# Kernel tuning notes

Hardware: AMD Instinct MI355X
Metric: run time of the kernel (lower is better)

Reference implementation:

```python
import jax, jax.numpy as jnp
import numpy as np

B, C, D, H, W = 4, 64, 64, 64, 64
EPS = 1e-5

def setup_inputs() -> dict:
    key = jax.random.key(0)
    ks = jax.random.split(key, 10)
    s = 1.0 / np.sqrt(C)
    so = 1.0 / np.sqrt(D)
    return {
        "x": jax.random.normal(ks[0], (B, C, H, W), jnp.float32),
        "gn_weight": jnp.ones((C,), jnp.float32),
        "gn_bias": jnp.zeros((C,), jnp.float32),
        "wq": jax.random.uniform(ks[1], (D, C), jnp.float32, -s, s),
        "bq": jax.random.uniform(ks[2], (D,), jnp.float32, -s, s),
        "wk": jax.random.uniform(ks[3], (D, C), jnp.float32, -s, s),
        "bk": jax.random.uniform(ks[4], (D,), jnp.float32, -s, s),
        "wv": jax.random.uniform(ks[5], (D, C), jnp.float32, -s, s),
        "bv": jax.random.uniform(ks[6], (D,), jnp.float32, -s, s),
        "wo": jax.random.uniform(ks[7], (D, D), jnp.float32, -so, so),
        "bo": jax.random.uniform(ks[8], (D,), jnp.float32, -so, so),
    }

def reference(x, gn_weight, gn_bias, wq, bq, wk, bk, wv, bv, wo, bo):
    # GroupNorm with num_groups == channels: per (batch, channel) norm over H,W
    mu = jnp.mean(x, axis=(2, 3), keepdims=True)
    var = jnp.var(x, axis=(2, 3), keepdims=True)
    xn = (x - mu) * jax.lax.rsqrt(var + EPS)
    xn = xn * gn_weight[None, :, None, None] + gn_bias[None, :, None, None]

    # 1x1 convs == channel matmuls; flatten spatial: bcn
    xf = xn.reshape(B, C, H * W)
    Q = jnp.einsum('dc,bcn->bdn', wq, xf) + bq[None, :, None]
    K = jnp.einsum('dc,bcn->bdn', wk, xf) + bk[None, :, None]
    V = jnp.einsum('dc,bcn->bdn', wv, xf) + bv[None, :, None]

    scale = 1.0 / jnp.sqrt(jnp.asarray(D, x.dtype))
    aff = jnp.einsum('bdn,bdm->bnm', Q, K) * scale  # [B, N, N]
    aff = jax.nn.softmax(aff, axis=2)
    att = jnp.einsum('bnm,bdm->bdn', aff, V)  # [B, D, N]

    out = jnp.einsum('ed,bdn->ben', wo, att) + bo[None, :, None]
    return out.reshape(B, D, H, W)
```

## Files before the change

### kernel.cpp

```cpp
#include <hip/hip_runtime.h>


#define B_ 4
#define C_ 64
#define D_ 64
#define N_ 4096

using bf16x8 = __attribute__((ext_vector_type(8))) short;
using u16x8  = __attribute__((ext_vector_type(8))) unsigned short;
using u32x4  = __attribute__((ext_vector_type(4))) unsigned int;
using f32x16 = __attribute__((ext_vector_type(16))) float;

__device__ __forceinline__ unsigned short f2bf(float f) {
    unsigned u = __builtin_bit_cast(unsigned, f);
    u = (u + 0x7FFFu + ((u >> 16) & 1u)) >> 16;
    return (unsigned short)u;
}

#if __has_builtin(__builtin_amdgcn_exp2f)
__device__ __forceinline__ float fast_exp2(float x) {
    return __builtin_amdgcn_exp2f(x);
}
#else
__device__ __forceinline__ float fast_exp2(float x) {
    float r;
    asm volatile("v_exp_f32 %0, %1\n\ts_nop 1" : "=v"(r) : "v"(x));
    return r;
}
#endif

__device__ __forceinline__ void gload16(const void* g, void* l) {
    __builtin_amdgcn_global_load_lds(
        (const __attribute__((address_space(1))) unsigned int*)g,
        (__attribute__((address_space(3))) unsigned int*)l, 16, 0, 0);
}

__global__ __launch_bounds__(1024)
void gn_stats_kernel(const float* __restrict__ x, float* __restrict__ stats) {
    __shared__ float red[32];
    const int bx  = blockIdx.x;
    const int tid = threadIdx.x;
    const float4* xp = (const float4*)(x + (size_t)bx * N_);
    float4 v = xp[tid];
    float s = (v.x + v.y) + (v.z + v.w);
    float q = (v.x * v.x + v.y * v.y) + (v.z * v.z + v.w * v.w);
#pragma unroll
    for (int off = 1; off < 64; off <<= 1) {
        s += __shfl_xor(s, off);
        q += __shfl_xor(q, off);
    }
    const int w = tid >> 6;
    if ((tid & 63) == 0) { red[w * 2] = s; red[w * 2 + 1] = q; }
    __syncthreads();
    if (w == 0) {
        const int lane = tid & 63;
        float sl = (lane < 16) ? red[lane * 2] : 0.f;
        float ql = (lane < 16) ? red[lane * 2 + 1] : 0.f;
#pragma unroll
        for (int off = 1; off < 16; off <<= 1) {
            sl += __shfl_xor(sl, off);
            ql += __shfl_xor(ql, off);
        }
        if (lane == 0) {
            float mu  = sl * (1.f / 4096.f);
            float var = ql * (1.f / 4096.f) - mu * mu;
            var = fmaxf(var, 0.f);
            stats[bx * 2]     = mu;
            stats[bx * 2 + 1] = 1.f / sqrtf(var + 1e-5f);
        }
    }
}

__global__ __launch_bounds__(512)
void gn_qkv_kernel(const float* __restrict__ x, const float* __restrict__ stats,
                   const float* __restrict__ gnw, const float* __restrict__ gnb,
                   const float* __restrict__ wq, const float* __restrict__ bq,
                   const float* __restrict__ wk, const float* __restrict__ bk,
                   const float* __restrict__ wv, const float* __restrict__ bv,
                   unsigned short* __restrict__ Qt, unsigned short* __restrict__ Kf,
                   unsigned short* __restrict__ Vf) {
    __shared__ float xn[64 * 64];
    __shared__ __align__(16) char vs[64 * 128];
    const int t  = threadIdx.x;
    const int bx = blockIdx.x;
    const int b  = bx >> 6;
    const int n0 = (bx & 63) * 64;

    {
        const int c  = t >> 3;
        const int nc = (t & 7) * 8;
        const float* xp = x + (size_t)(b * 64 + c) * N_ + n0 + nc;
        float4 xa = *(const float4*)(xp);
        float4 xb = *(const float4*)(xp + 4);
        float mu = stats[(b * 64 + c) * 2];
        float rs = stats[(b * 64 + c) * 2 + 1];
        float gw = gnw[c] * rs;
        float gb = gnb[c] - mu * gw;
        float* xr = xn + c * 64 + nc;
        xr[0] = xa.x * gw + gb; xr[1] = xa.y * gw + gb;
        xr[2] = xa.z * gw + gb; xr[3] = xa.w * gw + gb;
        xr[4] = xb.x * gw + gb; xr[5] = xb.y * gw + gb;
        xr[6] = xb.z * gw + gb; xr[7] = xb.w * gw + gb;
    }
    __syncthreads();

    const int n    = t & 63;
    const int dblk = __builtin_amdgcn_readfirstlane(t >> 6);
    const int d0   = dblk * 8;

    float aq[8], ak[8], av[8];
#pragma unroll
    for (int i = 0; i < 8; ++i) { aq[i] = 0.f; ak[i] = 0.f; av[i] = 0.f; }

#pragma unroll 4
    for (int c = 0; c < 64; ++c) {
        const float xv = xn[c * 64 + n];
#pragma unroll
        for (int i = 0; i < 8; ++i) {
            aq[i] += wq[(d0 + i) * 64 + c] * xv;
            ak[i] += wk[(d0 + i) * 64 + c] * xv;
            av[i] += wv[(d0 + i) * 64 + c] * xv;
        }
    }

    const float QS = 0.18033688011112042f;
    const int m = n0 + n;
    u16x8 qv, kv, vb;
#pragma unroll
    for (int i = 0; i < 8; ++i) {
        qv[i] = f2bf((aq[i] + bq[d0 + i]) * QS);
        kv[i] = f2bf(ak[i] + bk[d0 + i]);
        vb[i] = f2bf(av[i] + bv[d0 + i]);
    }
    *(u16x8*)(Qt + ((size_t)(b * N_ + m)) * 64 + d0) = qv;
    {
        const int kc = dblk >> 1, h = dblk & 1, mt = m >> 5;
        *(u16x8*)(Kf + ((size_t)((b * 128 + mt) * 4 + kc)) * 512
                     + (h * 32 + (m & 31)) * 8) = kv;
    }
    *(u16x8*)(vs + n * 128 + ((dblk * 16) ^ ((n & 7) << 4))) = vb;
    __syncthreads();

    {
        const int mc_l = t >> 7;
        const int dt   = (t >> 6) & 1;
        const int lp   = t & 63;
        const int hp   = lp >> 5;
        const int dcol = (lp & 31) + dt * 32;
        const int cbase = (dcol & ~7) * 2;
        const int clow  = (dcol & 7) * 2;
        u16x8 tmp;
#pragma unroll
        for (int j = 0; j < 8; ++j) {
            const int ml = mc_l * 16 + hp * 8 + j;
            tmp[j] = *(const unsigned short*)(
                vs + ml * 128 + (cbase ^ (j << 4)) + clow);
        }
        *(u16x8*)(Vf + ((size_t)((b * 256 + (n0 >> 4) + mc_l) * 2 + dt)) * 512
                     + lp * 8) = tmp;
    }
}

__global__ __launch_bounds__(512, 2)
void attn_kernel(const unsigned short* __restrict__ Qt,
                 const unsigned short* __restrict__ Kf,
                 const unsigned short* __restrict__ Vf,
                 const float* __restrict__ wo, const float* __restrict__ bo,
                 float* __restrict__ out) {
    __shared__ __align__(16) char smem[131072];
    const int tid  = threadIdx.x;
    const int lane = tid & 63;
    const int wvu  = __builtin_amdgcn_readfirstlane(tid >> 6);
    const int c    = lane & 31;
    const int h    = lane >> 5;
    const int bid  = blockIdx.x;
    const int b    = bid & 3;
    const int qc   = bid >> 2;
    const int n0   = qc * 64;

    const unsigned short* qp = Qt + (size_t)(b * N_ + n0 + c) * 64 + h * 8;
    bf16x8 qa0[4], qa1[4];
#pragma unroll
    for (int kc = 0; kc < 4; ++kc) {
        qa0[kc] = *(const bf16x8*)(qp + kc * 16);
        qa1[kc] = *(const bf16x8*)(qp + 32 * 64 + kc * 16);
    }

    f32x16 o00, o01, o10, o11;
#pragma unroll
    for (int i = 0; i < 16; ++i) { o00[i] = 0.f; o01[i] = 0.f; o10[i] = 0.f; o11[i] = 0.f; }
    float lsA0 = 0.f, lsA1 = 0.f, lsB0 = 0.f, lsB1 = 0.f;

    const int lof = lane * 16;
    char* sbase = smem + wvu * 16384;
    const char* kTn = (const char*)Kf + (size_t)b * 524288 + (size_t)wvu * 65536;
    const char* vTn = (const char*)Vf + (size_t)b * 524288 + (size_t)wvu * 65536;

#pragma unroll
    for (int j = 0; j < 4; ++j) {
        gload16(kTn + j * 1024 + lof, sbase + j * 1024);
        gload16(vTn + j * 1024 + lof, sbase + 4096 + j * 1024);
    }
    asm volatile("s_waitcnt vmcnt(0)" ::: "memory");
    __builtin_amdgcn_sched_barrier(0);

    for (int t = 0; t < 16; ++t) {
        char* buf = sbase + ((t & 1) << 13);
        if (t + 1 < 16) {
            kTn += 4096;
            vTn += 4096;
            char* dst = sbase + (((t & 1) ^ 1) << 13);
#pragma unroll
            for (int j = 0; j < 4; ++j) {
                gload16(kTn + j * 1024 + lof, dst + j * 1024);
                gload16(vTn + j * 1024 + lof, dst + 4096 + j * 1024);
            }
        }

        const char* kb = buf + lof;
        bf16x8 kf0 = *(const bf16x8*)(kb);
        bf16x8 kf1 = *(const bf16x8*)(kb + 1024);
        bf16x8 kf2 = *(const bf16x8*)(kb + 2048);
        bf16x8 kf3 = *(const bf16x8*)(kb + 3072);
        f32x16 sa0, sa1;
#pragma unroll
        for (int i = 0; i < 16; ++i) { sa0[i] = 0.f; sa1[i] = 0.f; }
        sa0 = __builtin_amdgcn_mfma_f32_32x32x16_bf16(kf0, qa0[0], sa0, 0, 0, 0);
        sa1 = __builtin_amdgcn_mfma_f32_32x32x16_bf16(kf0, qa1[0], sa1, 0, 0, 0);
        sa0 = __builtin_amdgcn_mfma_f32_32x32x16_bf16(kf1, qa0[1], sa0, 0, 0, 0);
        sa1 = __builtin_amdgcn_mfma_f32_32x32x16_bf16(kf1, qa1[1], sa1, 0, 0, 0);
        sa0 = __builtin_amdgcn_mfma_f32_32x32x16_bf16(kf2, qa0[2], sa0, 0, 0, 0);
        sa1 = __builtin_amdgcn_mfma_f32_32x32x16_bf16(kf2, qa1[2], sa1, 0, 0, 0);
        sa0 = __builtin_amdgcn_mfma_f32_32x32x16_bf16(kf3, qa0[3], sa0, 0, 0, 0);
        sa1 = __builtin_amdgcn_mfma_f32_32x32x16_bf16(kf3, qa1[3], sa1, 0, 0, 0);

#pragma unroll
        for (int i = 0; i < 16; i += 2) {
            float pA0 = fast_exp2(sa0[i]);
            float pA1 = fast_exp2(sa0[i + 1]);
            float pB0 = fast_exp2(sa1[i]);
            float pB1 = fast_exp2(sa1[i + 1]);
            sa0[i] = pA0; sa0[i + 1] = pA1;
            sa1[i] = pB0; sa1[i + 1] = pB1;
            lsA0 += pA0; lsA1 += pA1;
            lsB0 += pB0; lsB1 += pB1;
        }
        unsigned dwa[8], dwb[8];
#pragma unroll
        for (int i = 0; i < 8; ++i) {
            asm("v_cvt_pk_bf16_f32 %0, %1, %2"
                : "=v"(dwa[i]) : "v"(sa0[2 * i]), "v"(sa0[2 * i + 1]));
            asm("v_cvt_pk_bf16_f32 %0, %1, %2"
                : "=v"(dwb[i]) : "v"(sa1[2 * i]), "v"(sa1[2 * i + 1]));
        }
        asm("v_permlane32_swap_b32 %0, %1" : "+v"(dwa[0]), "+v"(dwa[2]));
        asm("v_permlane32_swap_b32 %0, %1" : "+v"(dwa[1]), "+v"(dwa[3]));
        asm("v_permlane32_swap_b32 %0, %1" : "+v"(dwa[4]), "+v"(dwa[6]));
        asm("v_permlane32_swap_b32 %0, %1" : "+v"(dwa[5]), "+v"(dwa[7]));
        asm("v_permlane32_swap_b32 %0, %1" : "+v"(dwb[0]), "+v"(dwb[2]));
        asm("v_permlane32_swap_b32 %0, %1" : "+v"(dwb[1]), "+v"(dwb[3]));
        asm("v_permlane32_swap_b32 %0, %1" : "+v"(dwb[4]), "+v"(dwb[6]));
        asm("v_permlane32_swap_b32 %0, %1" : "+v"(dwb[5]), "+v"(dwb[7]));
        bf16x8 pa0 = __builtin_bit_cast(bf16x8, (u32x4){dwa[0], dwa[1], dwa[2], dwa[3]});
        bf16x8 pa1 = __builtin_bit_cast(bf16x8, (u32x4){dwa[4], dwa[5], dwa[6], dwa[7]});
        bf16x8 pb0 = __builtin_bit_cast(bf16x8, (u32x4){dwb[0], dwb[1], dwb[2], dwb[3]});
        bf16x8 pb1 = __builtin_bit_cast(bf16x8, (u32x4){dwb[4], dwb[5], dwb[6], dwb[7]});

        const char* vbp = buf + 4096 + lof;
        bf16x8 vf0 = *(const bf16x8*)(vbp);
        bf16x8 vf1 = *(const bf16x8*)(vbp + 1024);
        bf16x8 vf2 = *(const bf16x8*)(vbp + 2048);
        bf16x8 vf3 = *(const bf16x8*)(vbp + 3072);
        o00 = __builtin_amdgcn_mfma_f32_32x32x16_bf16(vf0, pa0, o00, 0, 0, 0);
        o10 = __builtin_amdgcn_mfma_f32_32x32x16_bf16(vf0, pb0, o10, 0, 0, 0);
        o01 = __builtin_amdgcn_mfma_f32_32x32x16_bf16(vf1, pa0, o01, 0, 0, 0);
        o11 = __builtin_amdgcn_mfma_f32_32x32x16_bf16(vf1, pb0, o11, 0, 0, 0);
        o00 = __builtin_amdgcn_mfma_f32_32x32x16_bf16(vf2, pa1, o00, 0, 0, 0);
        o10 = __builtin_amdgcn_mfma_f32_32x32x16_bf16(vf2, pb1, o10, 0, 0, 0);
        o01 = __builtin_amdgcn_mfma_f32_32x32x16_bf16(vf3, pa1, o01, 0, 0, 0);
        o11 = __builtin_amdgcn_mfma_f32_32x32x16_bf16(vf3, pb1, o11, 0, 0, 0);

        asm volatile("s_waitcnt vmcnt(0)" ::: "memory");
        __builtin_amdgcn_sched_barrier(0);
    }

    float lsA = lsA0 + lsA1;
    float lsB = lsB0 + lsB1;
    float rsA = lsA + __shfl_xor(lsA, 32);
    float rsB = lsB + __shfl_xor(lsB, 32);

    __syncthreads();
    float* lsm   = (float*)(smem + 65536);
    float* atile = (float*)(smem + 68608);
    if (wvu < 4) {
        float* mrg = (float*)(smem + wvu * 16384);
#pragma unroll
        for (int r = 0; r < 16; ++r) {
            const int row = (r & 3) + 8 * (r >> 2) + 4 * h;
            mrg[row * 64 + c]             = o00[r];
            mrg[(row + 32) * 64 + c]      = o01[r];
            mrg[row * 64 + 32 + c]        = o10[r];
            mrg[(row + 32) * 64 + 32 + c] = o11[r];
        }
    }
    if (h == 0) {
        lsm[wvu * 64 + c]      = rsA;
        lsm[wvu * 64 + 32 + c] = rsB;
    }
    __syncthreads();
    if (wvu >= 4) {
        float* mrg = (float*)(smem + (wvu - 4) * 16384);
#pragma unroll
        for (int r = 0; r < 16; ++r) {
            const int row = (r & 3) + 8 * (r >> 2) + 4 * h;
            mrg[row * 64 + c]             += o00[r];
            mrg[(row + 32) * 64 + c]      += o01[r];
            mrg[row * 64 + 32 + c]        += o10[r];
            mrg[(row + 32) * 64 + 32 + c] += o11[r];
        }
    }
    __syncthreads();
    if (wvu < 4) {
        const int dh = wvu >> 1, qh = wvu & 1;
        const int qq = qh * 32 + c;
        float lt = 0.f;
#pragma unroll
        for (int k = 0; k < 8; ++k) lt += lsm[k * 64 + qq];
        const float inv = 1.f / lt;
        const float* m0 = (const float*)smem;
#pragma unroll
        for (int r = 0; r < 16; ++r) {
            const int row = dh * 32 + (r & 3) + 8 * (r >> 2) + 4 * h;
            const int idx = row * 64 + qq;
            float sum = (m0[idx] + m0[4096 + idx])
                      + (m0[8192 + idx] + m0[12288 + idx]);
            atile[row * 65 + qq] = sum * inv;
        }
    }
    __syncthreads();
    {
        const int n  = tid & 63;
        const int e0 = (tid >> 6) * 8;
        float acc[8];
#pragma unroll
        for (int i = 0; i < 8; ++i) acc[i] = bo[e0 + i];
#pragma unroll 8
        for (int d = 0; d < 64; ++d) {
            const float xv = atile[d * 65 + n];
#pragma unroll
            for (int i = 0; i < 8; ++i) acc[i] += wo[(e0 + i) * 64 + d] * xv;
        }
#pragma unroll
        for (int i = 0; i < 8; ++i)
            out[((size_t)(b * 64 + e0 + i) << 12) + n0 + n] = acc[i];
    }
}

extern "C" void kernel_launch(void* const* d_in, const int* in_sizes, int n_in,
                              void* d_out, int out_size, void* d_ws, size_t ws_size,
                              hipStream_t stream) {
    const float* x   = (const float*)d_in[0];
    const float* gnw = (const float*)d_in[1];
    const float* gnb = (const float*)d_in[2];
    const float* wq  = (const float*)d_in[3];
    const float* bq  = (const float*)d_in[4];
    const float* wk  = (const float*)d_in[5];
    const float* bk  = (const float*)d_in[6];
    const float* wv  = (const float*)d_in[7];
    const float* bv  = (const float*)d_in[8];
    const float* wo  = (const float*)d_in[9];
    const float* bo  = (const float*)d_in[10];
    float* out = (float*)d_out;

    char* wsb = (char*)d_ws;
    float*          stats = (float*)wsb;
    unsigned short* Qt    = (unsigned short*)(wsb + 2048);
    unsigned short* Kf    = (unsigned short*)(wsb + 2048 + 2097152);
    unsigned short* Vf    = (unsigned short*)(wsb + 2048 + 2 * 2097152);

    gn_stats_kernel<<<dim3(B_ * C_), dim3(1024), 0, stream>>>(x, stats);
    gn_qkv_kernel<<<dim3(B_ * 64), dim3(512), 0, stream>>>(
        x, stats, gnw, gnb, wq, bq, wk, bk, wv, bv, Qt, Kf, Vf);
    attn_kernel<<<dim3(B_ * 64), dim3(512), 0, stream>>>(
        Qt, Kf, Vf, wo, bo, out);
}
```

Baseline: 56.12 us.

## Halve attention query tile to 32 and double grid with single-buffered LDS

Each attention block now handles 32 queries instead of 64, and the grid doubles to 512 blocks so more of the GPU's compute units get work. LDS per block drops to 64KB by replacing double buffering with a single buffer: fragments are read into registers, then the next K/V tile is issued into the same slot. The epilogue is reworked for the smaller tile. The cost is that each K/V tile is read twice as many times overall, and the loads overlap less with compute because the single buffer forces a wait before every refill.

```diff
diff --git a/kernel.cpp b/kernel.cpp
--- a/kernel.cpp
+++ b/kernel.cpp
@@ -167,7 +167,7 @@
                  const unsigned short* __restrict__ Vf,
                  const float* __restrict__ wo, const float* __restrict__ bo,
                  float* __restrict__ out) {
-    __shared__ __align__(16) char smem[131072];
+    __shared__ __align__(16) char smem[65536];
     const int tid  = threadIdx.x;
     const int lane = tid & 63;
     const int wvu  = __builtin_amdgcn_readfirstlane(tid >> 6);
@@ -176,23 +176,20 @@
     const int bid  = blockIdx.x;
     const int b    = bid & 3;
     const int qc   = bid >> 2;
-    const int n0   = qc * 64;
+    const int n0   = qc * 32;
 
     const unsigned short* qp = Qt + (size_t)(b * N_ + n0 + c) * 64 + h * 8;
-    bf16x8 qa0[4], qa1[4];
-#pragma unroll
-    for (int kc = 0; kc < 4; ++kc) {
-        qa0[kc] = *(const bf16x8*)(qp + kc * 16);
-        qa1[kc] = *(const bf16x8*)(qp + 32 * 64 + kc * 16);
-    }
-
-    f32x16 o00, o01, o10, o11;
-#pragma unroll
-    for (int i = 0; i < 16; ++i) { o00[i] = 0.f; o01[i] = 0.f; o10[i] = 0.f; o11[i] = 0.f; }
-    float lsA0 = 0.f, lsA1 = 0.f, lsB0 = 0.f, lsB1 = 0.f;
+    bf16x8 qa[4];
+#pragma unroll
+    for (int kc = 0; kc < 4; ++kc) qa[kc] = *(const bf16x8*)(qp + kc * 16);
+
+    f32x16 oacc0, oacc1;
+#pragma unroll
+    for (int i = 0; i < 16; ++i) { oacc0[i] = 0.f; oacc1[i] = 0.f; }
+    float ls0 = 0.f, ls1 = 0.f;
 
     const int lof = lane * 16;
-    char* sbase = smem + wvu * 16384;
+    char* sbase = smem + wvu * 8192;
     const char* kTn = (const char*)Kf + (size_t)b * 524288 + (size_t)wvu * 65536;
     const char* vTn = (const char*)Vf + (size_t)b * 524288 + (size_t)wvu * 65536;
 
@@ -205,154 +202,130 @@
     __builtin_amdgcn_sched_barrier(0);
 
     for (int t = 0; t < 16; ++t) {
-        char* buf = sbase + ((t & 1) << 13);
-        if (t + 1 < 16) {
-            kTn += 4096;
-            vTn += 4096;
-            char* dst = sbase + (((t & 1) ^ 1) << 13);
-#pragma unroll
-            for (int j = 0; j < 4; ++j) {
-                gload16(kTn + j * 1024 + lof, dst + j * 1024);
-                gload16(vTn + j * 1024 + lof, dst + 4096 + j * 1024);
-            }
-        }
-
-        const char* kb = buf + lof;
+        const char* kb = sbase + lof;
         bf16x8 kf0 = *(const bf16x8*)(kb);
         bf16x8 kf1 = *(const bf16x8*)(kb + 1024);
         bf16x8 kf2 = *(const bf16x8*)(kb + 2048);
         bf16x8 kf3 = *(const bf16x8*)(kb + 3072);
-        f32x16 sa0, sa1;
-#pragma unroll
-        for (int i = 0; i < 16; ++i) { sa0[i] = 0.f; sa1[i] = 0.f; }
-        sa0 = __builtin_amdgcn_mfma_f32_32x32x16_bf16(kf0, qa0[0], sa0, 0, 0, 0);
-        sa1 = __builtin_amdgcn_mfma_f32_32x32x16_bf16(kf0, qa1[0], sa1, 0, 0, 0);
-        sa0 = __builtin_amdgcn_mfma_f32_32x32x16_bf16(kf1, qa0[1], sa0, 0, 0, 0);
-        sa1 = __builtin_amdgcn_mfma_f32_32x32x16_bf16(kf1, qa1[1], sa1, 0, 0, 0);
-        sa0 = __builtin_amdgcn_mfma_f32_32x32x16_bf16(kf2, qa0[2], sa0, 0, 0, 0);
-        sa1 = __builtin_amdgcn_mfma_f32_32x32x16_bf16(kf2, qa1[2], sa1, 0, 0, 0);
-        sa0 = __builtin_amdgcn_mfma_f32_32x32x16_bf16(kf3, qa0[3], sa0, 0, 0, 0);
-        sa1 = __builtin_amdgcn_mfma_f32_32x32x16_bf16(kf3, qa1[3], sa1, 0, 0, 0);
-
-#pragma unroll
-        for (int i = 0; i < 16; i += 2) {
-            float pA0 = fast_exp2(sa0[i]);
-            float pA1 = fast_exp2(sa0[i + 1]);
-            float pB0 = fast_exp2(sa1[i]);
-            float pB1 = fast_exp2(sa1[i + 1]);
-            sa0[i] = pA0; sa0[i + 1] = pA1;
-            sa1[i] = pB0; sa1[i + 1] = pB1;
-            lsA0 += pA0; lsA1 += pA1;
-            lsB0 += pB0; lsB1 += pB1;
-        }
-        unsigned dwa[8], dwb[8];
-#pragma unroll
-        for (int i = 0; i < 8; ++i) {
-            asm("v_cvt_pk_bf16_f32 %0, %1, %2"
-                : "=v"(dwa[i]) : "v"(sa0[2 * i]), "v"(sa0[2 * i + 1]));
-            asm("v_cvt_pk_bf16_f32 %0, %1, %2"
-                : "=v"(dwb[i]) : "v"(sa1[2 * i]), "v"(sa1[2 * i + 1]));
-        }
-        asm("v_permlane32_swap_b32 %0, %1" : "+v"(dwa[0]), "+v"(dwa[2]));
-        asm("v_permlane32_swap_b32 %0, %1" : "+v"(dwa[1]), "+v"(dwa[3]));
-        asm("v_permlane32_swap_b32 %0, %1" : "+v"(dwa[4]), "+v"(dwa[6]));
-        asm("v_permlane32_swap_b32 %0, %1" : "+v"(dwa[5]), "+v"(dwa[7]));
-        asm("v_permlane32_swap_b32 %0, %1" : "+v"(dwb[0]), "+v"(dwb[2]));
-        asm("v_permlane32_swap_b32 %0, %1" : "+v"(dwb[1]), "+v"(dwb[3]));
-        asm("v_permlane32_swap_b32 %0, %1" : "+v"(dwb[4]), "+v"(dwb[6]));
-        asm("v_permlane32_swap_b32 %0, %1" : "+v"(dwb[5]), "+v"(dwb[7]));
-        bf16x8 pa0 = __builtin_bit_cast(bf16x8, (u32x4){dwa[0], dwa[1], dwa[2], dwa[3]});
-        bf16x8 pa1 = __builtin_bit_cast(bf16x8, (u32x4){dwa[4], dwa[5], dwa[6], dwa[7]});
-        bf16x8 pb0 = __builtin_bit_cast(bf16x8, (u32x4){dwb[0], dwb[1], dwb[2], dwb[3]});
-        bf16x8 pb1 = __builtin_bit_cast(bf16x8, (u32x4){dwb[4], dwb[5], dwb[6], dwb[7]});
-
-        const char* vbp = buf + 4096 + lof;
+        const char* vbp = sbase + 4096 + lof;
         bf16x8 vf0 = *(const bf16x8*)(vbp);
         bf16x8 vf1 = *(const bf16x8*)(vbp + 1024);
         bf16x8 vf2 = *(const bf16x8*)(vbp + 2048);
         bf16x8 vf3 = *(const bf16x8*)(vbp + 3072);
-        o00 = __builtin_amdgcn_mfma_f32_32x32x16_bf16(vf0, pa0, o00, 0, 0, 0);
-        o10 = __builtin_amdgcn_mfma_f32_32x32x16_bf16(vf0, pb0, o10, 0, 0, 0);
-        o01 = __builtin_amdgcn_mfma_f32_32x32x16_bf16(vf1, pa0, o01, 0, 0, 0);
-        o11 = __builtin_amdgcn_mfma_f32_32x32x16_bf16(vf1, pb0, o11, 0, 0, 0);
-        o00 = __builtin_amdgcn_mfma_f32_32x32x16_bf16(vf2, pa1, o00, 0, 0, 0);
-        o10 = __builtin_amdgcn_mfma_f32_32x32x16_bf16(vf2, pb1, o10, 0, 0, 0);
-        o01 = __builtin_amdgcn_mfma_f32_32x32x16_bf16(vf3, pa1, o01, 0, 0, 0);
-        o11 = __builtin_amdgcn_mfma_f32_32x32x16_bf16(vf3, pb1, o11, 0, 0, 0);
+        asm volatile("s_waitcnt lgkmcnt(0)" ::: "memory");
+        __builtin_amdgcn_sched_barrier(0);
+
+        if (t + 1 < 16) {
+            kTn += 4096;
+            vTn += 4096;
+#pragma unroll
+            for (int j = 0; j < 4; ++j) {
+                gload16(kTn + j * 1024 + lof, sbase + j * 1024);
+                gload16(vTn + j * 1024 + lof, sbase + 4096 + j * 1024);
+            }
+        }
+
+        f32x16 sa;
+#pragma unroll
+        for (int i = 0; i < 16; ++i) sa[i] = 0.f;
+        sa = __builtin_amdgcn_mfma_f32_32x32x16_bf16(kf0, qa[0], sa, 0, 0, 0);
+        sa = __builtin_amdgcn_mfma_f32_32x32x16_bf16(kf1, qa[1], sa, 0, 0, 0);
+        sa = __builtin_amdgcn_mfma_f32_32x32x16_bf16(kf2, qa[2], sa, 0, 0, 0);
+        sa = __builtin_amdgcn_mfma_f32_32x32x16_bf16(kf3, qa[3], sa, 0, 0, 0);
+
+#pragma unroll
+        for (int i = 0; i < 16; i += 2) {
+            float p0 = fast_exp2(sa[i]);
+            float p1 = fast_exp2(sa[i + 1]);
+            sa[i] = p0; sa[i + 1] = p1;
+            ls0 += p0; ls1 += p1;
+        }
+        unsigned dw[8];
+#pragma unroll
+        for (int i = 0; i < 8; ++i)
+            asm("v_cvt_pk_bf16_f32 %0, %1, %2"
+                : "=v"(dw[i]) : "v"(sa[2 * i]), "v"(sa[2 * i + 1]));
+        asm("v_permlane32_swap_b32 %0, %1" : "+v"(dw[0]), "+v"(dw[2]));
+        asm("v_permlane32_swap_b32 %0, %1" : "+v"(dw[1]), "+v"(dw[3]));
+        asm("v_permlane32_swap_b32 %0, %1" : "+v"(dw[4]), "+v"(dw[6]));
+        asm("v_permlane32_swap_b32 %0, %1" : "+v"(dw[5]), "+v"(dw[7]));
+        bf16x8 pf0 = __builtin_bit_cast(bf16x8, (u32x4){dw[0], dw[1], dw[2], dw[3]});
+        bf16x8 pf1 = __builtin_bit_cast(bf16x8, (u32x4){dw[4], dw[5], dw[6], dw[7]});
+
+        oacc0 = __builtin_amdgcn_mfma_f32_32x32x16_bf16(vf0, pf0, oacc0, 0, 0, 0);
+        oacc1 = __builtin_amdgcn_mfma_f32_32x32x16_bf16(vf1, pf0, oacc1, 0, 0, 0);
+        oacc0 = __builtin_amdgcn_mfma_f32_32x32x16_bf16(vf2, pf1, oacc0, 0, 0, 0);
+        oacc1 = __builtin_amdgcn_mfma_f32_32x32x16_bf16(vf3, pf1, oacc1, 0, 0, 0);
 
         asm volatile("s_waitcnt vmcnt(0)" ::: "memory");
         __builtin_amdgcn_sched_barrier(0);
     }
 
-    float lsA = lsA0 + lsA1;
-    float lsB = lsB0 + lsB1;
-    float rsA = lsA + __shfl_xor(lsA, 32);
-    float rsB = lsB + __shfl_xor(lsB, 32);
-
-    __syncthreads();
-    float* lsm   = (float*)(smem + 65536);
-    float* atile = (float*)(smem + 68608);
+    float lsum = ls0 + ls1;
+    float rs = lsum + __shfl_xor(lsum, 32);
+
+    __syncthreads();
+    float* lsm   = (float*)(smem + 32768);
+    float* invl  = (float*)(smem + 33792);
+    float* atile = (float*)(smem + 33920);
     if (wvu < 4) {
-        float* mrg = (float*)(smem + wvu * 16384);
+        float* mrg = (float*)(smem + wvu * 8192);
 #pragma unroll
         for (int r = 0; r < 16; ++r) {
             const int row = (r & 3) + 8 * (r >> 2) + 4 * h;
-            mrg[row * 64 + c]             = o00[r];
-            mrg[(row + 32) * 64 + c]      = o01[r];
-            mrg[row * 64 + 32 + c]        = o10[r];
-            mrg[(row + 32) * 64 + 32 + c] = o11[r];
-        }
-    }
-    if (h == 0) {
-        lsm[wvu * 64 + c]      = rsA;
-        lsm[wvu * 64 + 32 + c] = rsB;
-    }
+            mrg[row * 32 + c]        = oacc0[r];
+            mrg[(row + 32) * 32 + c] = oacc1[r];
+        }
+    }
+    if (h == 0) lsm[wvu * 32 + c] = rs;
     __syncthreads();
     if (wvu >= 4) {
-        float* mrg = (float*)(smem + (wvu - 4) * 16384);
+        float* mrg = (float*)(smem + (wvu - 4) * 8192);
 #pragma unroll
         for (int r = 0; r < 16; ++r) {
             const int row = (r & 3) + 8 * (r >> 2) + 4 * h;
-            mrg[row * 64 + c]             += o00[r];
-            mrg[(row + 32) * 64 + c]      += o01[r];
-            mrg[row * 64 + 32 + c]        += o10[r];
-            mrg[(row + 32) * 64 + 32 + c] += o11[r];
-        }
-    }
-    __syncthreads();
-    if (wvu < 4) {
-        const int dh = wvu >> 1, qh = wvu & 1;
-        const int qq = qh * 32 + c;
+            mrg[row * 32 + c]        += oacc0[r];
+            mrg[(row + 32) * 32 + c] += oacc1[r];
+        }
+    }
+    if (tid < 32) {
+    }
+    __syncthreads();
+    if (tid < 32) {
         float lt = 0.f;
 #pragma unroll
-        for (int k = 0; k < 8; ++k) lt += lsm[k * 64 + qq];
-        const float inv = 1.f / lt;
+        for (int k = 0; k < 8; ++k) lt += lsm[k * 32 + tid];
+        invl[tid] = 1.f / lt;
+    }
+    __syncthreads();
+    {
         const float* m0 = (const float*)smem;
 #pragma unroll
-        for (int r = 0; r < 16; ++r) {
-            const int row = dh * 32 + (r & 3) + 8 * (r >> 2) + 4 * h;
-            const int idx = row * 64 + qq;
-            float sum = (m0[idx] + m0[4096 + idx])
-                      + (m0[8192 + idx] + m0[12288 + idx]);
-            atile[row * 65 + qq] = sum * inv;
-        }
-    }
-    __syncthreads();
-    {
-        const int n  = tid & 63;
-        const int e0 = (tid >> 6) * 8;
-        float acc[8];
-#pragma unroll
-        for (int i = 0; i < 8; ++i) acc[i] = bo[e0 + i];
+        for (int k = 0; k < 4; ++k) {
+            const int idx = k * 512 + tid;
+            const int d   = idx >> 5;
+            const int q   = idx & 31;
+            float sum = (m0[idx] + m0[2048 + idx])
+                      + (m0[4096 + idx] + m0[6144 + idx]);
+            atile[d * 33 + q] = sum * invl[q];
+        }
+    }
+    __syncthreads();
+    {
+        const int q  = tid & 31;
+        const int e0 = (tid >> 5) * 4;
+        float acc[4];
+#pragma unroll
+        for (int i = 0; i < 4; ++i) acc[i] = bo[e0 + i];
 #pragma unroll 8
         for (int d = 0; d < 64; ++d) {
-            const float xv = atile[d * 65 + n];
-#pragma unroll
-            for (int i = 0; i < 8; ++i) acc[i] += wo[(e0 + i) * 64 + d] * xv;
-        }
-#pragma unroll
-        for (int i = 0; i < 8; ++i)
-            out[((size_t)(b * 64 + e0 + i) << 12) + n0 + n] = acc[i];
+            const float xv = atile[d * 33 + q];
+#pragma unroll
+            for (int i = 0; i < 4; ++i) acc[i] += wo[(e0 + i) * 64 + d] * xv;
+        }
+#pragma unroll
+        for (int i = 0; i < 4; ++i)
+            out[((size_t)(b * 64 + e0 + i) << 12) + n0 + q] = acc[i];
     }
 }
 
@@ -381,6 +354,6 @@
     gn_stats_kernel<<<dim3(B_ * C_), dim3(1024), 0, stream>>>(x, stats);
     gn_qkv_kernel<<<dim3(B_ * 64), dim3(512), 0, stream>>>(
         x, stats, gnw, gnb, wq, bq, wk, bk, wv, bv, Qt, Kf, Vf);
-    attn_kernel<<<dim3(B_ * 64), dim3(512), 0, stream>>>(
+    attn_kernel<<<dim3(B_ * 128), dim3(512), 0, stream>>>(
         Qt, Kf, Vf, wo, bo, out);
 }
```

After: 59.21 us. 1.06x slower.
